# Kernel tuning notes

Measured on AMD Instinct MI355X. Metric: run time of the kernel, lower is better.

Reference implementation:

```python
import jax, jax.numpy as jnp
import numpy as np

N_NODES = 10000
N_EDGES = 160000
MUL = 16          # multiplicity (num_radial channels) per irrep
EMB = 64          # radial_embed_size
HID = 128         # radial_hidden_size
N_PATHS = 5       # (0,0,0),(1,1,0),(0,1,1),(1,0,1),(1,1,1)
W_NUMEL = N_PATHS * MUL * MUL  # 1280


def setup_inputs() -> dict:
    key = jax.random.key(0)
    ks = jax.random.split(key, 9)
    return {
        'edge_index': jax.random.randint(ks[0], (2, N_EDGES), 0, N_NODES),
        'node_feat': jax.random.normal(ks[1], (N_NODES, 4 * MUL), dtype=jnp.float32),
        'edge_feat': jax.random.normal(ks[2], (N_EDGES, 4), dtype=jnp.float32),
        'edge_embed': jax.random.normal(ks[3], (N_EDGES, EMB), dtype=jnp.float32),
        'fc_w1': jax.random.normal(ks[4], (EMB, HID), dtype=jnp.float32),
        'fc_w2': jax.random.normal(ks[5], (HID, HID), dtype=jnp.float32),
        'fc_w3': jax.random.normal(ks[6], (HID, W_NUMEL), dtype=jnp.float32),
        'sc_w0': jax.random.normal(ks[7], (MUL, MUL), dtype=jnp.float32),
        'sc_w1': jax.random.normal(ks[8], (MUL, MUL), dtype=jnp.float32),
    }


def reference(edge_index, node_feat, edge_feat, edge_embed,
              fc_w1, fc_w2, fc_w3, sc_w0, sc_w1):
    """InfGCN GCNLayer: gather src features, fully-connected e3nn-style tensor
    product (irreps '16x0e+16x1o' x SH '1x0e+1x1o' -> '16x0e+16x1o') with
    per-edge weights from a radial MLP, scatter-add into dst, plus o3.Linear
    self-connection. e3nn conventions: FullyConnectedNet normalizes each layer
    by 1/sqrt(fan_in), component irrep_normalization gives w3j factors 1/sqrt(3)
    (1x1->0 dot) and 1/sqrt(2) (1x1->1 cross), element path_normalization gives
    per-path 1/sqrt(mul_in)."""
    E = edge_embed.shape[0]
    N = node_feat.shape[0]
    src, dst = edge_index[0], edge_index[1]

    # radial network (silu on hidden layers, e3nn fan-in normalization)
    h = jax.nn.silu(edge_embed @ (fc_w1 / np.sqrt(EMB)))
    h = jax.nn.silu(h @ (fc_w2 / np.sqrt(HID)))
    w = (h @ (fc_w3 / np.sqrt(HID))).reshape(E, N_PATHS, MUL, MUL)  # [E,P,u,w]

    # gather + split src features into l=0 / l=1 parts
    x = node_feat[src]                       # [E, 64]
    x0 = x[:, :MUL]                          # [E, u]
    x1 = x[:, MUL:].reshape(E, MUL, 3)       # [E, u, 3]
    y0 = edge_feat[:, :1]                    # [E, 1]
    y1 = edge_feat[:, 1:4]                   # [E, 3]

    inv = 1.0 / np.sqrt(MUL)                 # path fan-in normalization
    # l=0 output: paths (0,0,0) and (1,1,0)
    dot = jnp.einsum('eud,ed->eu', x1, y1) / np.sqrt(3.0)
    o0 = (jnp.einsum('euw,eu->ew', w[:, 0], x0 * y0)
          + jnp.einsum('euw,eu->ew', w[:, 1], dot)) * inv     # [E, w]
    # l=1 output: paths (0,1,1), (1,0,1), (1,1,1)
    cross = jnp.cross(x1, y1[:, None, :]) / np.sqrt(2.0)       # [E, u, 3]
    o1 = (jnp.einsum('euw,eu,ed->ewd', w[:, 2], x0, y1)
          + jnp.einsum('euw,eud->ewd', w[:, 3], x1 * y0[:, :, None])
          + jnp.einsum('euw,eud->ewd', w[:, 4], cross)) * inv  # [E, w, 3]

    msg = jnp.concatenate([o0, o1.reshape(E, 3 * MUL)], axis=-1)  # [E, 64]
    out = jax.ops.segment_sum(msg, dst, num_segments=N)            # [N, 64]

    # self-connection: o3.Linear, per-l channel mixing
    s0 = (node_feat[:, :MUL] @ sc_w0) * inv
    s1 = jnp.einsum('nud,uw->nwd', node_feat[:, MUL:].reshape(N, MUL, 3), sc_w1) * inv
    return out + jnp.concatenate([s0, s1.reshape(N, 3 * MUL)], axis=-1)
```

## Files before the change

kernel.cpp:

```cpp
#include <hip/hip_runtime.h>

#define NNODES 10000
#define NEDGES 160000
#define MUL 16
#define EMB 64
#define HID 128

#define RS128 0.08838834764831845f
#define SC3   (0.08838834764831845f * 0.25f)

typedef __attribute__((ext_vector_type(8))) _Float16 half8;
typedef __attribute__((ext_vector_type(4))) _Float16 half4;
typedef __attribute__((ext_vector_type(4))) float f32x4;

__global__ __launch_bounds__(256) void selfconn_kernel(
    const float* __restrict__ node_feat,
    const float* __restrict__ sc_w0,
    const float* __restrict__ sc_w1,
    float* __restrict__ out)
{
    const int tid = threadIdx.x;
    const int nl = tid >> 4;
    const int wp = tid & 15;
    const int n  = blockIdx.x * 16 + nl;

    __shared__ float nf[16][64];
    __shared__ float w0s[16][16];
    __shared__ float w1s[16][16];

    ((float4*)nf)[tid] = ((const float4*)(node_feat + (size_t)blockIdx.x * 16 * 64))[tid];
    if (tid < 64)       ((float4*)w0s)[tid]      = ((const float4*)sc_w0)[tid];
    else if (tid < 128) ((float4*)w1s)[tid - 64] = ((const float4*)sc_w1)[tid - 64];
    __syncthreads();

    float o0 = 0.f, o1x = 0.f, o1y = 0.f, o1z = 0.f;
#pragma unroll
    for (int u = 0; u < 16; ++u) {
        o0 += nf[nl][u] * w0s[u][wp];
        const float wv = w1s[u][wp];
        o1x += nf[nl][16 + u * 3 + 0] * wv;
        o1y += nf[nl][16 + u * 3 + 1] * wv;
        o1z += nf[nl][16 + u * 3 + 2] * wv;
    }
    float* op = out + (size_t)n * 64;
    op[wp]              = o0  * 0.25f;
    op[16 + wp * 3 + 0] = o1x * 0.25f;
    op[16 + wp * 3 + 1] = o1y * 0.25f;
    op[16 + wp * 3 + 2] = o1z * 0.25f;
}

__global__ __launch_bounds__(256) void prep_kernel(
    const float* __restrict__ w1,
    const float* __restrict__ w2,
    const float* __restrict__ w3,
    _Float16* __restrict__ wp)
{
    int idx = blockIdx.x * 256 + threadIdx.x;
    if (idx < 8192) {
        int j = idx & 7, lane = (idx >> 3) & 63, ks = (idx >> 9) & 1, nt = idx >> 10;
        int k = ks * 32 + (lane >> 4) * 8 + j;
        int n = nt * 16 + (lane & 15);
        wp[idx] = (_Float16)(w1[k * HID + n] * 0.125f);
    } else if (idx < 24576) {
        int t = idx - 8192;
        int j = t & 7, lane = (t >> 3) & 63, ks = (t >> 9) & 3, nt = t >> 11;
        int k = ks * 32 + (lane >> 4) * 8 + j;
        int n = nt * 16 + (lane & 15);
        wp[idx] = (_Float16)(w2[k * HID + n] * RS128);
    } else if (idx < 188416) {
        int t = idx - 24576;
        int j = t & 7, lane = (t >> 3) & 63, ks = (t >> 9) & 3, nt = t >> 11;
        int k = ks * 32 + (lane >> 4) * 8 + j;
        int n = nt * 16 + (lane & 15);
        wp[idx] = (_Float16)(w3[k * 1280 + n] * SC3);
    }
}

__global__ __launch_bounds__(256, 3) void edge_mfma_kernel(
    const int*   __restrict__ ei,
    const float* __restrict__ node_feat,
    const float* __restrict__ edge_feat,
    const float* __restrict__ edge_embed,
    const _Float16* __restrict__ wpk,
    float* __restrict__ out)
{
    const int tid = threadIdx.x;
    const int e0  = blockIdx.x * 32;

    __shared__ __align__(16) char eeRaw[32 * 128];
    __shared__ __align__(16) char h1Raw[32 * 256];
    __shared__ __align__(16) char h2Raw[32 * 256];
    __shared__ float sA [32][17];
    __shared__ float sB [32][17];
    __shared__ float sX0[32][17];
    __shared__ float sP3[32][49];
    __shared__ float sP4[32][49];
    __shared__ float sY1[32][5];
    __shared__ float opart[32][48];
    __shared__ float sEF[32][4];
    __shared__ int   sidx[64];

    if (tid < 32)       sidx[tid] = ei[e0 + tid];
    else if (tid < 64)  sidx[tid] = ei[NEDGES + e0 + (tid - 32)];
    else if (tid < 192) {
        int t = tid - 64;
        sEF[t >> 2][t & 3] = edge_feat[(e0 + (t >> 2)) * 4 + (t & 3)];
    }
    __syncthreads();

    float* xg = (float*)h1Raw;
    {
        const float4* eesrc = (const float4*)(edge_embed + (size_t)e0 * EMB);
#pragma unroll
        for (int it = 0; it < 2; ++it) {
            int f = tid + it * 256;
            int row = f >> 4, c4 = f & 15;
            float4 v = eesrc[f];
            half4 h = { (_Float16)v.x, (_Float16)v.y, (_Float16)v.z, (_Float16)v.w };
            *(half4*)(eeRaw + row * 128 + ((c4 * 8) ^ ((row & 7) << 4))) = h;

            int src = sidx[row];
            float4 nv = ((const float4*)(node_feat + (size_t)src * 64))[c4];
            ((float4*)(xg + row * 64))[c4] = nv;
        }
    }
    __syncthreads();

#pragma unroll
    for (int it = 0; it < 2; ++it) {
        int el = (tid >> 4) + it * 16;
        int u  = tid & 15;
        const float* xr = xg + el * 64;
        float x0u = xr[u];
        float xa  = xr[16 + u * 3 + 0];
        float xb  = xr[16 + u * 3 + 1];
        float xc  = xr[16 + u * 3 + 2];
        float y0  = sEF[el][0];
        float y1x = sEF[el][1];
        float y1y = sEF[el][2];
        float y1z = sEF[el][3];
        sX0[el][u] = x0u;
        sA [el][u] = x0u * y0;
        sB [el][u] = (xa * y1x + xb * y1y + xc * y1z) * 0.5773502691896258f;
        sP3[el][u * 3 + 0] = xa * y0;
        sP3[el][u * 3 + 1] = xb * y0;
        sP3[el][u * 3 + 2] = xc * y0;
        sP4[el][u * 3 + 0] = (xb * y1z - xc * y1y) * 0.7071067811865476f;
        sP4[el][u * 3 + 1] = (xc * y1x - xa * y1z) * 0.7071067811865476f;
        sP4[el][u * 3 + 2] = (xa * y1y - xb * y1x) * 0.7071067811865476f;
        if (u == 0) { sY1[el][0] = y1x; sY1[el][1] = y1y; sY1[el][2] = y1z; }
    }
    __syncthreads();

    const int lane  = tid & 63;
    const int w     = tid >> 6;
    const int wm    = w & 1;
    const int wn    = w >> 1;
    const int arow  = wm * 16 + (lane & 15);
    const int aswz  = (arow & 7) << 4;
    const int ako2  = ((lane >> 4) * 8) * 2;
    const int crow0 = wm * 16 + (lane >> 4) * 4;
    const int ccol  = lane & 15;

    const half8* w1p8 = (const half8*)wpk;
    const half8* w2p8 = (const half8*)(wpk + 8192);
    const half8* w3p8 = (const half8*)(wpk + 24576);
    _Float16* h1s = (_Float16*)h1Raw;
    _Float16* h2s = (_Float16*)h2Raw;

    {
        half8 a0 = *(const half8*)(eeRaw + arow * 128 + ((ako2     ) ^ aswz));
        half8 a1 = *(const half8*)(eeRaw + arow * 128 + ((64 + ako2) ^ aswz));
#pragma unroll
        for (int i = 0; i < 4; ++i) {
            int nt = wn * 4 + i;
            f32x4 c = {0.f, 0.f, 0.f, 0.f};
            c = __builtin_amdgcn_mfma_f32_16x16x32_f16(a0, w1p8[(nt * 2 + 0) * 64 + lane], c, 0, 0, 0);
            c = __builtin_amdgcn_mfma_f32_16x16x32_f16(a1, w1p8[(nt * 2 + 1) * 64 + lane], c, 0, 0, 0);
#pragma unroll
            for (int r = 0; r < 4; ++r) {
                int row = crow0 + r;
                int col = nt * 16 + ccol;
                float x = c[r];
                float s = x / (1.f + __expf(-x));
                *(_Float16*)(h1Raw + row * 256 + ((col * 2) ^ ((row & 7) << 4))) = (_Float16)s;
            }
        }
    }
    __syncthreads();

    {
        half8 a2[4];
#pragma unroll
        for (int ks = 0; ks < 4; ++ks)
            a2[ks] = *(const half8*)(h1Raw + arow * 256 + ((ks * 64 + ako2) ^ aswz));
#pragma unroll
        for (int i = 0; i < 4; ++i) {
            int nt = wn * 4 + i;
            f32x4 c = {0.f, 0.f, 0.f, 0.f};
#pragma unroll
            for (int ks = 0; ks < 4; ++ks)
                c = __builtin_amdgcn_mfma_f32_16x16x32_f16(a2[ks], w2p8[(nt * 4 + ks) * 64 + lane], c, 0, 0, 0);
#pragma unroll
            for (int r = 0; r < 4; ++r) {
                int row = crow0 + r;
                int col = nt * 16 + ccol;
                float x = c[r];
                float s = x / (1.f + __expf(-x));
                *(_Float16*)(h2Raw + row * 256 + ((col * 2) ^ ((row & 7) << 4))) = (_Float16)s;
            }
        }
    }
    __syncthreads();

    half8 a3[4];
#pragma unroll
    for (int ks = 0; ks < 4; ++ks)
        a3[ks] = *(const half8*)(h2Raw + arow * 256 + ((ks * 64 + ako2) ^ aswz));

    float acc0[4] = {0.f, 0.f, 0.f, 0.f};
    float acc1[4][3] = {{0.f,0.f,0.f},{0.f,0.f,0.f},{0.f,0.f,0.f},{0.f,0.f,0.f}};

#define MM_TILE(NT, C)                                                          \
    { const half8* bp = w3p8 + ((NT) * 4) * 64 + lane;                          \
      C = __builtin_amdgcn_mfma_f32_16x16x32_f16(a3[0], bp[0],   C, 0, 0, 0);   \
      C = __builtin_amdgcn_mfma_f32_16x16x32_f16(a3[1], bp[64],  C, 0, 0, 0);   \
      C = __builtin_amdgcn_mfma_f32_16x16x32_f16(a3[2], bp[128], C, 0, 0, 0);   \
      C = __builtin_amdgcn_mfma_f32_16x16x32_f16(a3[3], bp[192], C, 0, 0, 0); }

    if (wn == 0) {
#pragma unroll 4
        for (int u = 0; u < 16; ++u) {
            f32x4 c = {0.f, 0.f, 0.f, 0.f};
            MM_TILE(u, c);
#pragma unroll
            for (int r = 0; r < 4; ++r) acc0[r] += c[r] * sA[crow0 + r][u];
        }
#pragma unroll 4
        for (int u = 0; u < 16; ++u) {
            f32x4 c = {0.f, 0.f, 0.f, 0.f};
            MM_TILE(16 + u, c);
#pragma unroll
            for (int r = 0; r < 4; ++r) acc0[r] += c[r] * sB[crow0 + r][u];
        }
#pragma unroll 4
        for (int u = 0; u < 8; ++u) {
            f32x4 c = {0.f, 0.f, 0.f, 0.f};
            MM_TILE(32 + u, c);
#pragma unroll
            for (int r = 0; r < 4; ++r) {
                float t = c[r] * sX0[crow0 + r][u];
#pragma unroll
                for (int d = 0; d < 3; ++d) acc1[r][d] += t * sY1[crow0 + r][d];
            }
        }
    } else {
#pragma unroll 4
        for (int u = 8; u < 16; ++u) {
            f32x4 c = {0.f, 0.f, 0.f, 0.f};
            MM_TILE(32 + u, c);
#pragma unroll
            for (int r = 0; r < 4; ++r) {
                float t = c[r] * sX0[crow0 + r][u];
#pragma unroll
                for (int d = 0; d < 3; ++d) acc1[r][d] += t * sY1[crow0 + r][d];
            }
        }
#pragma unroll 4
        for (int u = 0; u < 16; ++u) {
            f32x4 c = {0.f, 0.f, 0.f, 0.f};
            MM_TILE(48 + u, c);
#pragma unroll
            for (int r = 0; r < 4; ++r)
#pragma unroll
                for (int d = 0; d < 3; ++d) acc1[r][d] += c[r] * sP3[crow0 + r][u * 3 + d];
        }
#pragma unroll 4
        for (int u = 0; u < 16; ++u) {
            f32x4 c = {0.f, 0.f, 0.f, 0.f};
            MM_TILE(64 + u, c);
#pragma unroll
            for (int r = 0; r < 4; ++r)
#pragma unroll
                for (int d = 0; d < 3; ++d) acc1[r][d] += c[r] * sP4[crow0 + r][u * 3 + d];
        }
    }
#undef MM_TILE

    if (wn == 0) {
#pragma unroll
        for (int r = 0; r < 4; ++r)
#pragma unroll
            for (int d = 0; d < 3; ++d)
                opart[crow0 + r][ccol * 3 + d] = acc1[r][d];
    }
    __syncthreads();

    if (wn == 0) {
#pragma unroll
        for (int r = 0; r < 4; ++r) {
            int el = crow0 + r;
            int dst = sidx[32 + el];
            atomicAdd(&out[(size_t)dst * 64 + ccol], acc0[r]);
        }
    } else {
#pragma unroll
        for (int r = 0; r < 4; ++r) {
            int el = crow0 + r;
            int dst = sidx[32 + el];
#pragma unroll
            for (int d = 0; d < 3; ++d)
                atomicAdd(&out[(size_t)dst * 64 + 16 + ccol * 3 + d],
                          acc1[r][d] + opart[el][ccol * 3 + d]);
        }
    }
}

extern "C" void kernel_launch(void* const* d_in, const int* in_sizes, int n_in,
                              void* d_out, int out_size, void* d_ws, size_t ws_size,
                              hipStream_t stream) {
    const int*   ei         = (const int*)  d_in[0];
    const float* node_feat  = (const float*)d_in[1];
    const float* edge_feat  = (const float*)d_in[2];
    const float* edge_embed = (const float*)d_in[3];
    const float* fc_w1      = (const float*)d_in[4];
    const float* fc_w2      = (const float*)d_in[5];
    const float* fc_w3      = (const float*)d_in[6];
    const float* sc_w0      = (const float*)d_in[7];
    const float* sc_w1      = (const float*)d_in[8];
    float* out = (float*)d_out;
    _Float16* wpk = (_Float16*)d_ws;

    prep_kernel<<<736, 256, 0, stream>>>(fc_w1, fc_w2, fc_w3, wpk);
    selfconn_kernel<<<NNODES / 16, 256, 0, stream>>>(node_feat, sc_w0, sc_w1, out);
    edge_mfma_kernel<<<NEDGES / 32, 256, 0, stream>>>(ei, node_feat, edge_feat, edge_embed,
                                                      wpk, out);
}
```

Before: 157.2 us.

## Rebalance layer-3 MFMA across waves with shared B fragments and smem reduction

Each wave now computes both 16-row M tiles, so each loaded w3 B fragment feeds two MFMAs, halving global weight fragment loads per block. The 80 N-tiles are split evenly across the four waves (20 each) rather than by wave halves. The epilogue scalars are stored transposed in shared memory so they can be read as float4. Partial outputs from all four waves are reduced through a padded shared buffer before the atomics, and shared memory is consolidated into one aliased buffer with launch bounds raised to 4 blocks per CU. In exchange, register pressure rises from double-sized A fragments and accumulators, and an extra shared-memory reduction pass with a sync is added.

```diff
diff --git a/kernel.cpp b/kernel.cpp
--- a/kernel.cpp
+++ b/kernel.cpp
@@ -76,7 +76,21 @@
     }
 }
 
-__global__ __launch_bounds__(256, 3) void edge_mfma_kernel(
+#define EE_OFF   0
+#define H1_OFF   4096
+#define H2_OFF   12288
+#define SA_OFF   20480
+#define SB_OFF   22528
+#define SX_OFF   24576
+#define SP3_OFF  26624
+#define SP4_OFF  32768
+#define SY_OFF   38912
+#define SEF_OFF  39296
+#define SIDX_OFF 39808
+#define SMEM_BYTES 40064
+#define OPW 65
+
+__global__ __launch_bounds__(256, 4) void edge_mfma_kernel(
     const int*   __restrict__ ei,
     const float* __restrict__ node_feat,
     const float* __restrict__ edge_feat,
@@ -84,31 +98,23 @@
     const _Float16* __restrict__ wpk,
     float* __restrict__ out)
 {
+    __shared__ __align__(16) char smem[SMEM_BYTES];
+
     const int tid = threadIdx.x;
     const int e0  = blockIdx.x * 32;
 
-    __shared__ __align__(16) char eeRaw[32 * 128];
-    __shared__ __align__(16) char h1Raw[32 * 256];
-    __shared__ __align__(16) char h2Raw[32 * 256];
-    __shared__ float sA [32][17];
-    __shared__ float sB [32][17];
-    __shared__ float sX0[32][17];
-    __shared__ float sP3[32][49];
-    __shared__ float sP4[32][49];
-    __shared__ float sY1[32][5];
-    __shared__ float opart[32][48];
-    __shared__ float sEF[32][4];
-    __shared__ int   sidx[64];
-
-    if (tid < 32)       sidx[tid] = ei[e0 + tid];
-    else if (tid < 64)  sidx[tid] = ei[NEDGES + e0 + (tid - 32)];
+    int*   sidxp = (int*)(smem + SIDX_OFF);
+    float* sEFp  = (float*)(smem + SEF_OFF);
+
+    if (tid < 32)       sidxp[tid] = ei[e0 + tid];
+    else if (tid < 64)  sidxp[tid] = ei[NEDGES + e0 + (tid - 32)];
     else if (tid < 192) {
         int t = tid - 64;
-        sEF[t >> 2][t & 3] = edge_feat[(e0 + (t >> 2)) * 4 + (t & 3)];
-    }
-    __syncthreads();
-
-    float* xg = (float*)h1Raw;
+        sEFp[t] = edge_feat[e0 * 4 + t];
+    }
+    __syncthreads();
+
+    float* xg = (float*)(smem + H1_OFF);
     {
         const float4* eesrc = (const float4*)(edge_embed + (size_t)e0 * EMB);
 #pragma unroll
@@ -117,38 +123,46 @@
             int row = f >> 4, c4 = f & 15;
             float4 v = eesrc[f];
             half4 h = { (_Float16)v.x, (_Float16)v.y, (_Float16)v.z, (_Float16)v.w };
-            *(half4*)(eeRaw + row * 128 + ((c4 * 8) ^ ((row & 7) << 4))) = h;
-
-            int src = sidx[row];
+            *(half4*)(smem + EE_OFF + row * 128 + ((c4 * 8) ^ ((row & 7) << 4))) = h;
+
+            int src = sidxp[row];
             float4 nv = ((const float4*)(node_feat + (size_t)src * 64))[c4];
             ((float4*)(xg + row * 64))[c4] = nv;
         }
     }
     __syncthreads();
 
-#pragma unroll
-    for (int it = 0; it < 2; ++it) {
-        int el = (tid >> 4) + it * 16;
-        int u  = tid & 15;
-        const float* xr = xg + el * 64;
-        float x0u = xr[u];
-        float xa  = xr[16 + u * 3 + 0];
-        float xb  = xr[16 + u * 3 + 1];
-        float xc  = xr[16 + u * 3 + 2];
-        float y0  = sEF[el][0];
-        float y1x = sEF[el][1];
-        float y1y = sEF[el][2];
-        float y1z = sEF[el][3];
-        sX0[el][u] = x0u;
-        sA [el][u] = x0u * y0;
-        sB [el][u] = (xa * y1x + xb * y1y + xc * y1z) * 0.5773502691896258f;
-        sP3[el][u * 3 + 0] = xa * y0;
-        sP3[el][u * 3 + 1] = xb * y0;
-        sP3[el][u * 3 + 2] = xc * y0;
-        sP4[el][u * 3 + 0] = (xb * y1z - xc * y1y) * 0.7071067811865476f;
-        sP4[el][u * 3 + 1] = (xc * y1x - xa * y1z) * 0.7071067811865476f;
-        sP4[el][u * 3 + 2] = (xa * y1y - xb * y1x) * 0.7071067811865476f;
-        if (u == 0) { sY1[el][0] = y1x; sY1[el][1] = y1y; sY1[el][2] = y1z; }
+    {
+        float* sAT  = (float*)(smem + SA_OFF);
+        float* sBT  = (float*)(smem + SB_OFF);
+        float* sXT  = (float*)(smem + SX_OFF);
+        float* sP3T = (float*)(smem + SP3_OFF);
+        float* sP4T = (float*)(smem + SP4_OFF);
+        float* sYT  = (float*)(smem + SY_OFF);
+#pragma unroll
+        for (int it = 0; it < 2; ++it) {
+            int el = (tid >> 4) + it * 16;
+            int u  = tid & 15;
+            const float* xr = xg + el * 64;
+            float x0u = xr[u];
+            float xa  = xr[16 + u * 3 + 0];
+            float xb  = xr[16 + u * 3 + 1];
+            float xc  = xr[16 + u * 3 + 2];
+            float y0  = sEFp[el * 4 + 0];
+            float y1x = sEFp[el * 4 + 1];
+            float y1y = sEFp[el * 4 + 2];
+            float y1z = sEFp[el * 4 + 3];
+            sXT[u * 32 + el] = x0u;
+            sAT[u * 32 + el] = x0u * y0;
+            sBT[u * 32 + el] = (xa * y1x + xb * y1y + xc * y1z) * 0.5773502691896258f;
+            sP3T[u * 96 + el * 3 + 0] = xa * y0;
+            sP3T[u * 96 + el * 3 + 1] = xb * y0;
+            sP3T[u * 96 + el * 3 + 2] = xc * y0;
+            sP4T[u * 96 + el * 3 + 0] = (xb * y1z - xc * y1y) * 0.7071067811865476f;
+            sP4T[u * 96 + el * 3 + 1] = (xc * y1x - xa * y1z) * 0.7071067811865476f;
+            sP4T[u * 96 + el * 3 + 2] = (xa * y1y - xb * y1x) * 0.7071067811865476f;
+            if (u < 3) sYT[u * 32 + el] = sEFp[el * 4 + 1 + u];
+        }
     }
     __syncthreads();
 
@@ -156,21 +170,20 @@
     const int w     = tid >> 6;
     const int wm    = w & 1;
     const int wn    = w >> 1;
-    const int arow  = wm * 16 + (lane & 15);
-    const int aswz  = (arow & 7) << 4;
-    const int ako2  = ((lane >> 4) * 8) * 2;
-    const int crow0 = wm * 16 + (lane >> 4) * 4;
+    const int aswz  = (lane & 7) << 4;
+    const int ako2  = (lane >> 4) * 16;
     const int ccol  = lane & 15;
+    const int crow00 = (lane >> 4) * 4;
 
     const half8* w1p8 = (const half8*)wpk;
     const half8* w2p8 = (const half8*)(wpk + 8192);
     const half8* w3p8 = (const half8*)(wpk + 24576);
-    _Float16* h1s = (_Float16*)h1Raw;
-    _Float16* h2s = (_Float16*)h2Raw;
-
-    {
-        half8 a0 = *(const half8*)(eeRaw + arow * 128 + ((ako2     ) ^ aswz));
-        half8 a1 = *(const half8*)(eeRaw + arow * 128 + ((64 + ako2) ^ aswz));
+
+    {
+        const int arow = wm * 16 + (lane & 15);
+        half8 a0 = *(const half8*)(smem + EE_OFF + arow * 128 + ((ako2     ) ^ aswz));
+        half8 a1 = *(const half8*)(smem + EE_OFF + arow * 128 + ((64 + ako2) ^ aswz));
+        const int crow0 = wm * 16 + crow00;
 #pragma unroll
         for (int i = 0; i < 4; ++i) {
             int nt = wn * 4 + i;
@@ -183,17 +196,19 @@
                 int col = nt * 16 + ccol;
                 float x = c[r];
                 float s = x / (1.f + __expf(-x));
-                *(_Float16*)(h1Raw + row * 256 + ((col * 2) ^ ((row & 7) << 4))) = (_Float16)s;
+                *(_Float16*)(smem + H1_OFF + row * 256 + ((col * 2) ^ ((row & 7) << 4))) = (_Float16)s;
             }
         }
     }
     __syncthreads();
 
     {
+        const int arow = wm * 16 + (lane & 15);
         half8 a2[4];
 #pragma unroll
         for (int ks = 0; ks < 4; ++ks)
-            a2[ks] = *(const half8*)(h1Raw + arow * 256 + ((ks * 64 + ako2) ^ aswz));
+            a2[ks] = *(const half8*)(smem + H1_OFF + arow * 256 + ((ks * 64 + ako2) ^ aswz));
+        const int crow0 = wm * 16 + crow00;
 #pragma unroll
         for (int i = 0; i < 4; ++i) {
             int nt = wn * 4 + i;
@@ -207,111 +222,154 @@
                 int col = nt * 16 + ccol;
                 float x = c[r];
                 float s = x / (1.f + __expf(-x));
-                *(_Float16*)(h2Raw + row * 256 + ((col * 2) ^ ((row & 7) << 4))) = (_Float16)s;
+                *(_Float16*)(smem + H2_OFF + row * 256 + ((col * 2) ^ ((row & 7) << 4))) = (_Float16)s;
             }
         }
     }
     __syncthreads();
 
-    half8 a3[4];
-#pragma unroll
-    for (int ks = 0; ks < 4; ++ks)
-        a3[ks] = *(const half8*)(h2Raw + arow * 256 + ((ks * 64 + ako2) ^ aswz));
-
-    float acc0[4] = {0.f, 0.f, 0.f, 0.f};
-    float acc1[4][3] = {{0.f,0.f,0.f},{0.f,0.f,0.f},{0.f,0.f,0.f},{0.f,0.f,0.f}};
-
-#define MM_TILE(NT, C)                                                          \
-    { const half8* bp = w3p8 + ((NT) * 4) * 64 + lane;                          \
-      C = __builtin_amdgcn_mfma_f32_16x16x32_f16(a3[0], bp[0],   C, 0, 0, 0);   \
-      C = __builtin_amdgcn_mfma_f32_16x16x32_f16(a3[1], bp[64],  C, 0, 0, 0);   \
-      C = __builtin_amdgcn_mfma_f32_16x16x32_f16(a3[2], bp[128], C, 0, 0, 0);   \
-      C = __builtin_amdgcn_mfma_f32_16x16x32_f16(a3[3], bp[192], C, 0, 0, 0); }
-
-    if (wn == 0) {
-#pragma unroll 4
-        for (int u = 0; u < 16; ++u) {
-            f32x4 c = {0.f, 0.f, 0.f, 0.f};
-            MM_TILE(u, c);
-#pragma unroll
-            for (int r = 0; r < 4; ++r) acc0[r] += c[r] * sA[crow0 + r][u];
-        }
-#pragma unroll 4
-        for (int u = 0; u < 16; ++u) {
-            f32x4 c = {0.f, 0.f, 0.f, 0.f};
-            MM_TILE(16 + u, c);
-#pragma unroll
-            for (int r = 0; r < 4; ++r) acc0[r] += c[r] * sB[crow0 + r][u];
-        }
-#pragma unroll 4
-        for (int u = 0; u < 8; ++u) {
-            f32x4 c = {0.f, 0.f, 0.f, 0.f};
-            MM_TILE(32 + u, c);
+    half8 a3[2][4];
+#pragma unroll
+    for (int m = 0; m < 2; ++m) {
+        const int arow = m * 16 + (lane & 15);
+#pragma unroll
+        for (int ks = 0; ks < 4; ++ks)
+            a3[m][ks] = *(const half8*)(smem + H2_OFF + arow * 256 + ((ks * 64 + ako2) ^ aswz));
+    }
+
+    float acc0[2][4] = {{0,0,0,0},{0,0,0,0}};
+    float s2  [2][4] = {{0,0,0,0},{0,0,0,0}};
+    float acc1[2][4][3] = {};
+
+#define MM8(NT, C0, C1) { \
+    const half8* bp = w3p8 + (size_t)(NT) * 256 + lane; \
+    half8 b0 = bp[0], b1 = bp[64], b2 = bp[128], b3 = bp[192]; \
+    C0 = __builtin_amdgcn_mfma_f32_16x16x32_f16(a3[0][0], b0, C0, 0, 0, 0); \
+    C1 = __builtin_amdgcn_mfma_f32_16x16x32_f16(a3[1][0], b0, C1, 0, 0, 0); \
+    C0 = __builtin_amdgcn_mfma_f32_16x16x32_f16(a3[0][1], b1, C0, 0, 0, 0); \
+    C1 = __builtin_amdgcn_mfma_f32_16x16x32_f16(a3[1][1], b1, C1, 0, 0, 0); \
+    C0 = __builtin_amdgcn_mfma_f32_16x16x32_f16(a3[0][2], b2, C0, 0, 0, 0); \
+    C1 = __builtin_amdgcn_mfma_f32_16x16x32_f16(a3[1][2], b2, C1, 0, 0, 0); \
+    C0 = __builtin_amdgcn_mfma_f32_16x16x32_f16(a3[0][3], b3, C0, 0, 0, 0); \
+    C1 = __builtin_amdgcn_mfma_f32_16x16x32_f16(a3[1][3], b3, C1, 0, 0, 0); }
+
+#define EPI_T(U, TOFF, ACC) { \
+    float4 t0 = *(const float4*)(smem + (TOFF) + (U) * 128 + crow00 * 4); \
+    float4 t1 = *(const float4*)(smem + (TOFF) + (U) * 128 + crow00 * 4 + 64); \
+    ACC[0][0] += c0[0] * t0.x; ACC[0][1] += c0[1] * t0.y; \
+    ACC[0][2] += c0[2] * t0.z; ACC[0][3] += c0[3] * t0.w; \
+    ACC[1][0] += c1[0] * t1.x; ACC[1][1] += c1[1] * t1.y; \
+    ACC[1][2] += c1[2] * t1.z; ACC[1][3] += c1[3] * t1.w; }
+
+#define EPI_V(U, TOFF) { \
+    const char* tb = smem + (TOFF) + (U) * 384 + crow00 * 12; \
+    float4 q0 = *(const float4*)(tb);      \
+    float4 q1 = *(const float4*)(tb + 16); \
+    float4 q2 = *(const float4*)(tb + 32); \
+    acc1[0][0][0] += c0[0]*q0.x; acc1[0][0][1] += c0[0]*q0.y; acc1[0][0][2] += c0[0]*q0.z; \
+    acc1[0][1][0] += c0[1]*q0.w; acc1[0][1][1] += c0[1]*q1.x; acc1[0][1][2] += c0[1]*q1.y; \
+    acc1[0][2][0] += c0[2]*q1.z; acc1[0][2][1] += c0[2]*q1.w; acc1[0][2][2] += c0[2]*q2.x; \
+    acc1[0][3][0] += c0[3]*q2.y; acc1[0][3][1] += c0[3]*q2.z; acc1[0][3][2] += c0[3]*q2.w; \
+    float4 p0 = *(const float4*)(tb + 192); \
+    float4 p1 = *(const float4*)(tb + 208); \
+    float4 p2 = *(const float4*)(tb + 224); \
+    acc1[1][0][0] += c1[0]*p0.x; acc1[1][0][1] += c1[0]*p0.y; acc1[1][0][2] += c1[0]*p0.z; \
+    acc1[1][1][0] += c1[1]*p0.w; acc1[1][1][1] += c1[1]*p1.x; acc1[1][1][2] += c1[1]*p1.y; \
+    acc1[1][2][0] += c1[2]*p1.z; acc1[1][2][1] += c1[2]*p1.w; acc1[1][2][2] += c1[2]*p2.x; \
+    acc1[1][3][0] += c1[3]*p2.y; acc1[1][3][1] += c1[3]*p2.z; acc1[1][3][2] += c1[3]*p2.w; }
+
+#define TILE_T(NT, U, TOFF, ACC) { \
+    f32x4 c0 = {0.f,0.f,0.f,0.f}, c1 = {0.f,0.f,0.f,0.f}; \
+    MM8(NT, c0, c1); EPI_T(U, TOFF, ACC); }
+
+#define TILE_V(NT, U, TOFF) { \
+    f32x4 c0 = {0.f,0.f,0.f,0.f}, c1 = {0.f,0.f,0.f,0.f}; \
+    MM8(NT, c0, c1); EPI_V(U, TOFF); }
+
+    switch (w) {
+    case 0:
+#pragma unroll 4
+        for (int u = 0; u < 16; ++u) TILE_T(u, u, SA_OFF, acc0);
+#pragma unroll
+        for (int u = 0; u < 4; ++u)  TILE_T(16 + u, u, SB_OFF, acc0);
+        break;
+    case 1:
+#pragma unroll 4
+        for (int u = 4; u < 16; ++u) TILE_T(16 + u, u, SB_OFF, acc0);
+#pragma unroll 4
+        for (int u = 0; u < 8; ++u)  TILE_T(32 + u, u, SX_OFF, s2);
+        break;
+    case 2:
+#pragma unroll 4
+        for (int u = 8; u < 16; ++u) TILE_T(32 + u, u, SX_OFF, s2);
+#pragma unroll 4
+        for (int u = 0; u < 12; ++u) TILE_V(48 + u, u, SP3_OFF);
+        break;
+    default:
+#pragma unroll
+        for (int u = 12; u < 16; ++u) TILE_V(48 + u, u, SP3_OFF);
+#pragma unroll 4
+        for (int u = 0; u < 16; ++u)  TILE_V(64 + u, u, SP4_OFF);
+        break;
+    }
+#undef MM8
+#undef EPI_T
+#undef EPI_V
+#undef TILE_T
+#undef TILE_V
+
+#pragma unroll
+    for (int m = 0; m < 2; ++m) {
+        const char* yb = smem + SY_OFF + crow00 * 4 + m * 64;
+        float4 yx = *(const float4*)(yb);
+        float4 yy = *(const float4*)(yb + 128);
+        float4 yz = *(const float4*)(yb + 256);
+        acc1[m][0][0] += s2[m][0] * yx.x; acc1[m][0][1] += s2[m][0] * yy.x; acc1[m][0][2] += s2[m][0] * yz.x;
+        acc1[m][1][0] += s2[m][1] * yx.y; acc1[m][1][1] += s2[m][1] * yy.y; acc1[m][1][2] += s2[m][1] * yz.y;
+        acc1[m][2][0] += s2[m][2] * yx.z; acc1[m][2][1] += s2[m][2] * yy.z; acc1[m][2][2] += s2[m][2] * yz.z;
+        acc1[m][3][0] += s2[m][3] * yx.w; acc1[m][3][1] += s2[m][3] * yy.w; acc1[m][3][2] += s2[m][3] * yz.w;
+    }
+
+    __syncthreads();
+
+    {
+        float* myop = (float*)smem + w * 32 * OPW;
+#pragma unroll
+        for (int m = 0; m < 2; ++m)
 #pragma unroll
             for (int r = 0; r < 4; ++r) {
-                float t = c[r] * sX0[crow0 + r][u];
-#pragma unroll
-                for (int d = 0; d < 3; ++d) acc1[r][d] += t * sY1[crow0 + r][d];
+                int row = crow00 + m * 16 + r;
+                float* rp = myop + row * OPW;
+                rp[ccol]                 = acc0[m][r];
+                rp[16 + ccol * 3 + 0]    = acc1[m][r][0];
+                rp[16 + ccol * 3 + 1]    = acc1[m][r][1];
+                rp[16 + ccol * 3 + 2]    = acc1[m][r][2];
             }
-        }
-    } else {
-#pragma unroll 4
-        for (int u = 8; u < 16; ++u) {
-            f32x4 c = {0.f, 0.f, 0.f, 0.f};
-            MM_TILE(32 + u, c);
-#pragma unroll
-            for (int r = 0; r < 4; ++r) {
-                float t = c[r] * sX0[crow0 + r][u];
-#pragma unroll
-                for (int d = 0; d < 3; ++d) acc1[r][d] += t * sY1[crow0 + r][d];
+    }
+    __syncthreads();
+
+    {
+        const float* opf = (const float*)smem;
+        const int rloc = lane >> 4;
+#pragma unroll
+        for (int rr = 0; rr < 2; ++rr) {
+            int row = w * 8 + rr * 4 + rloc;
+            int dst = sidxp[32 + row];
+            float* op = out + (size_t)dst * 64;
+            float v = opf[0 * 32 * OPW + row * OPW + ccol]
+                    + opf[1 * 32 * OPW + row * OPW + ccol]
+                    + opf[2 * 32 * OPW + row * OPW + ccol]
+                    + opf[3 * 32 * OPW + row * OPW + ccol];
+            atomicAdd(op + ccol, v);
+#pragma unroll
+            for (int d = 0; d < 3; ++d) {
+                int c = 16 + ccol * 3 + d;
+                float v1 = opf[0 * 32 * OPW + row * OPW + c]
+                         + opf[1 * 32 * OPW + row * OPW + c]
+                         + opf[2 * 32 * OPW + row * OPW + c]
+                         + opf[3 * 32 * OPW + row * OPW + c];
+                atomicAdd(op + c, v1);
             }
-        }
-#pragma unroll 4
-        for (int u = 0; u < 16; ++u) {
-            f32x4 c = {0.f, 0.f, 0.f, 0.f};
-            MM_TILE(48 + u, c);
-#pragma unroll
-            for (int r = 0; r < 4; ++r)
-#pragma unroll
-                for (int d = 0; d < 3; ++d) acc1[r][d] += c[r] * sP3[crow0 + r][u * 3 + d];
-        }
-#pragma unroll 4
-        for (int u = 0; u < 16; ++u) {
-            f32x4 c = {0.f, 0.f, 0.f, 0.f};
-            MM_TILE(64 + u, c);
-#pragma unroll
-            for (int r = 0; r < 4; ++r)
-#pragma unroll
-                for (int d = 0; d < 3; ++d) acc1[r][d] += c[r] * sP4[crow0 + r][u * 3 + d];
-        }
-    }
-#undef MM_TILE
-
-    if (wn == 0) {
-#pragma unroll
-        for (int r = 0; r < 4; ++r)
-#pragma unroll
-            for (int d = 0; d < 3; ++d)
-                opart[crow0 + r][ccol * 3 + d] = acc1[r][d];
-    }
-    __syncthreads();
-
-    if (wn == 0) {
-#pragma unroll
-        for (int r = 0; r < 4; ++r) {
-            int el = crow0 + r;
-            int dst = sidx[32 + el];
-            atomicAdd(&out[(size_t)dst * 64 + ccol], acc0[r]);
-        }
-    } else {
-#pragma unroll
-        for (int r = 0; r < 4; ++r) {
-            int el = crow0 + r;
-            int dst = sidx[32 + el];
-#pragma unroll
-            for (int d = 0; d < 3; ++d)
-                atomicAdd(&out[(size_t)dst * 64 + 16 + ccol * 3 + d],
-                          acc1[r][d] + opart[el][ccol * 3 + d]);
         }
     }
 }
```

Measured after the change: 149.0 us. -5.2%, faster.
